# Kernel tuning notes

Measured on AMD Instinct MI355X. Metric: run time of the kernel, lower is better.

The kernel has to match this reference:

```python
import jax, jax.numpy as jnp
import numpy as np

N_NODES = 100000
N_EDGES = 1600000
D_IN = 128
D_OUT = 128
NEG_SLOPE = 0.01  # torch F.leaky_relu default


def setup_inputs() -> dict:
    key = jax.random.key(0)
    k1, k2, k3, k4, k5 = jax.random.split(key, 5)
    h = jax.random.normal(k1, (N_NODES, D_IN), dtype=jnp.float32)
    # nn.Linear default init scale ~ 1/sqrt(fan_in)
    W = jax.random.normal(k2, (D_IN, D_OUT), dtype=jnp.float32) / np.sqrt(D_IN)
    attn_w = jax.random.normal(k3, (2 * D_OUT,), dtype=jnp.float32) / np.sqrt(2 * D_OUT)
    edge_src = jax.random.randint(k4, (N_EDGES,), 0, N_NODES, dtype=jnp.int32)
    edge_dst = jax.random.randint(k5, (N_EDGES,), 0, N_NODES, dtype=jnp.int32)
    return {"h": h, "W": W, "attn_w": attn_w, "edge_src": edge_src, "edge_dst": edge_dst}


def reference(h, W, attn_w, edge_src, edge_dst):
    n = h.shape[0]
    d = W.shape[1]
    z = h @ W                                   # [N, d]
    # attention_func(cat([z_src, z_dst])) == z_src @ a[:d] + z_dst @ a[d:]
    s_src = z @ attn_w[:d]                      # [N]
    s_dst = z @ attn_w[d:]                      # [N]
    e = jax.nn.leaky_relu(s_src[edge_src] + s_dst[edge_dst], NEG_SLOPE)  # [E]
    # segment softmax over incoming edges of each dst node
    m = jax.ops.segment_max(e, edge_dst, num_segments=n)   # [N], -inf for empty
    ex = jnp.exp(e - m[edge_dst])                           # [E]
    denom = jax.ops.segment_sum(ex, edge_dst, num_segments=n)  # [N]
    alpha = ex / denom[edge_dst]                             # [E]
    # weighted neighbor sum: sum_j alpha_ij * z_j
    out = jax.ops.segment_sum(alpha[:, None] * z[edge_src], edge_dst, num_segments=n)
    return out
```

## Files before the change

### kernel.cpp

```cpp
#include <hip/hip_runtime.h>

#define D 128
#define NEG_SLOPE 0.01f
#define BSHIFT 7
#define B1 1024
#define STR 136
#define SCHUNK 4096
#define SLOT 2560

typedef __attribute__((ext_vector_type(8))) short short8;
typedef __attribute__((ext_vector_type(4))) float floatx4;

__device__ __forceinline__ unsigned f2bf_rne(float x) {
    unsigned u = __float_as_uint(x);
    return (u + 0x7fffu + ((u >> 16) & 1u)) >> 16;
}
#define BF_LO(u) __uint_as_float((u) << 16)
#define BF_HI(u) __uint_as_float((u) & 0xffff0000u)

__global__ void init_gcur(int* __restrict__ gcur) {
    const int i = threadIdx.x;
    gcur[i] = i * SLOT;
}

__global__ __launch_bounds__(1024) void sort_scatter(const int* __restrict__ esrc,
                                                     const int* __restrict__ edst,
                                                     int* __restrict__ gcur,
                                                     int* __restrict__ pairs, int E) {
    __shared__ int cnt[B1], exc[B1], gbs[B1], cur[B1];
    __shared__ int spk[SCHUNK];
    __shared__ unsigned short sbkt[SCHUNK];
    const int t = threadIdx.x;
    cnt[t] = 0; cur[t] = 0;
    __syncthreads();

    const int e0 = blockIdx.x * SCHUNK;
    const int n  = min(SCHUNK, E - e0);

    int pk[4], bk[4];
#pragma unroll
    for (int k = 0; k < 4; ++k) {
        const int i = t + k * 1024;
        if (i < n) {
            const int d = edst[e0 + i];
            const int s = esrc[e0 + i];
            bk[k] = d >> BSHIFT;
            pk[k] = (s << BSHIFT) | (d & 127);
            atomicAdd(&cnt[bk[k]], 1);
        } else {
            bk[k] = -1;
        }
    }
    __syncthreads();

    exc[t] = cnt[t];
    __syncthreads();
    for (int off = 1; off < B1; off <<= 1) {
        int v = (t >= off) ? exc[t - off] : 0;
        __syncthreads();
        exc[t] += v;
        __syncthreads();
    }
    const int myexc = exc[t] - cnt[t];
    exc[t] = myexc;
    if (cnt[t] > 0) gbs[t] = atomicAdd(&gcur[t], cnt[t]);
    __syncthreads();

#pragma unroll
    for (int k = 0; k < 4; ++k) {
        if (bk[k] >= 0) {
            const int p = exc[bk[k]] + atomicAdd(&cur[bk[k]], 1);
            spk[p]  = pk[k];
            sbkt[p] = (unsigned short)bk[k];
        }
    }
    __syncthreads();

    for (int i = t; i < n; i += 1024) {
        const int b = sbkt[i];
        const int pos = gbs[b] + (i - exc[b]);
        if (pos < (b + 1) * SLOT) pairs[pos] = spk[i];
    }
}

__global__ __launch_bounds__(256) void fine_build(const int* __restrict__ pairs,
                                                  const int* __restrict__ gcur,
                                                  int* __restrict__ beg,
                                                  int* __restrict__ ncnt,
                                                  int* __restrict__ adj, int N) {
    __shared__ int cnt[128], sc[128], cur[128];
    const int b = blockIdx.x;
    const int base = b << BSHIFT;
    const int nd = min(128, N - base);
    const int t = threadIdx.x;
    const int s0 = b * SLOT;
    const int e1 = min(gcur[b], s0 + SLOT);
    if (t < 128) { cnt[t] = 0; cur[t] = 0; }
    __syncthreads();
    for (int i = s0 + t; i < e1; i += 256)
        atomicAdd(&cnt[pairs[i] & 127], 1);
    __syncthreads();
    if (t < 128) sc[t] = cnt[t];
    __syncthreads();
    for (int off = 1; off < 128; off <<= 1) {
        int v = (t < 128 && t >= off) ? sc[t - off] : 0;
        __syncthreads();
        if (t < 128) sc[t] += v;
        __syncthreads();
    }
    if (t < nd) {
        beg[base + t]  = s0 + sc[t] - cnt[t];
        ncnt[base + t] = cnt[t];
    }
    __syncthreads();
    for (int i = s0 + t; i < e1; i += 256) {
        const int pkv = pairs[i];
        const int d = pkv & 127;
        const int pos = s0 + (sc[d] - cnt[d]) + atomicAdd(&cur[d], 1);
        adj[pos] = pkv >> BSHIFT;
    }
}

__global__ __launch_bounds__(256) void gemm_zs(const float* __restrict__ h,
                                               const float* __restrict__ W,
                                               const float* __restrict__ aw,
                                               unsigned short* __restrict__ z,
                                               float* __restrict__ s_src,
                                               float* __restrict__ s_dst, int N) {
    __shared__ unsigned short ws_hi[D * STR];
    __shared__ unsigned short ws_lo[D * STR];
    const int t = threadIdx.x;
    for (int i = t; i < D * D; i += 256) {
        int k = i >> 7, n = i & 127;
        float x = W[i];
        unsigned hi = f2bf_rne(x);
        float hf = __uint_as_float(hi << 16);
        unsigned lo = __float_as_uint(x - hf) >> 16;
        ws_hi[n * STR + k] = (unsigned short)hi;
        ws_lo[n * STR + k] = (unsigned short)lo;
    }
    __syncthreads();

    const int lane = t & 63, quad = lane >> 4, l16 = lane & 15;
    const int rowbase = blockIdx.x * 64 + (t >> 6) * 16;
    const int arow = min(rowbase + l16, N - 1);
    const float* __restrict__ hrow = h + (size_t)arow * D;

    floatx4 acc[8];
#pragma unroll
    for (int ct = 0; ct < 8; ++ct) acc[ct] = (floatx4){0.f, 0.f, 0.f, 0.f};

#pragma unroll
    for (int kk = 0; kk < 4; ++kk) {
        const int k0 = kk * 32 + quad * 8;
        float4 x0 = *(const float4*)&hrow[k0];
        float4 x1 = *(const float4*)&hrow[k0 + 4];
        float xs[8] = {x0.x, x0.y, x0.z, x0.w, x1.x, x1.y, x1.z, x1.w};
        union { short8 v; unsigned short u[8]; } ahi, alo;
#pragma unroll
        for (int i = 0; i < 8; ++i) {
            unsigned hi = f2bf_rne(xs[i]);
            float hf = __uint_as_float(hi << 16);
            ahi.u[i] = (unsigned short)hi;
            alo.u[i] = (unsigned short)(__float_as_uint(xs[i] - hf) >> 16);
        }
#pragma unroll
        for (int ct = 0; ct < 8; ++ct) {
            const int bo = (ct * 16 + l16) * STR + k0;
            short8 bhi = *(const short8*)&ws_hi[bo];
            short8 blo = *(const short8*)&ws_lo[bo];
            acc[ct] = __builtin_amdgcn_mfma_f32_16x16x32_bf16(ahi.v, bhi, acc[ct], 0, 0, 0);
            acc[ct] = __builtin_amdgcn_mfma_f32_16x16x32_bf16(alo.v, bhi, acc[ct], 0, 0, 0);
            acc[ct] = __builtin_amdgcn_mfma_f32_16x16x32_bf16(ahi.v, blo, acc[ct], 0, 0, 0);
        }
    }

#pragma unroll
    for (int ct = 0; ct < 8; ++ct)
#pragma unroll
        for (int reg = 0; reg < 4; ++reg) {
            int r = rowbase + quad * 4 + reg;
            if (r < N)
                z[(size_t)r * D + ct * 16 + l16] = (unsigned short)f2bf_rne(acc[ct][reg]);
        }

    float ps[4] = {0.f, 0.f, 0.f, 0.f}, pd[4] = {0.f, 0.f, 0.f, 0.f};
#pragma unroll
    for (int ct = 0; ct < 8; ++ct) {
        float as = aw[ct * 16 + l16];
        float ad = aw[128 + ct * 16 + l16];
#pragma unroll
        for (int reg = 0; reg < 4; ++reg) {
            ps[reg] = fmaf(acc[ct][reg], as, ps[reg]);
            pd[reg] = fmaf(acc[ct][reg], ad, pd[reg]);
        }
    }
#pragma unroll
    for (int reg = 0; reg < 4; ++reg)
#pragma unroll
        for (int o = 1; o < 16; o <<= 1) {
            ps[reg] += __shfl_xor(ps[reg], o, 64);
            pd[reg] += __shfl_xor(pd[reg], o, 64);
        }
    if (l16 == 0) {
#pragma unroll
        for (int reg = 0; reg < 4; ++reg) {
            int r = rowbase + quad * 4 + reg;
            if (r < N) { s_src[r] = ps[reg]; s_dst[r] = pd[reg]; }
        }
    }
}

__global__ __launch_bounds__(256) void aggregate(const unsigned short* __restrict__ z,
                                                 const float* __restrict__ s_src,
                                                 const float* __restrict__ s_dst,
                                                 const int* __restrict__ beg_,
                                                 const int* __restrict__ ncnt_,
                                                 const int* __restrict__ adj,
                                                 float* __restrict__ out, int N) {
    const int lane = threadIdx.x & 63;
    const int q    = lane >> 4;
    const int l16  = lane & 15;
    const int node = blockIdx.x * 4 + (threadIdx.x >> 6);
    if (node >= N) return;
    const int beg = beg_[node];
    const int cnt = ncnt_[node];
    const float sd = s_dst[node];

    float a[8] = {0.f,0.f,0.f,0.f,0.f,0.f,0.f,0.f};
    float bacc[8] = {0.f,0.f,0.f,0.f,0.f,0.f,0.f,0.f};

    auto fma8 = [&](float* ac, float w, const uint4& v) {
        ac[0] = fmaf(w, BF_LO(v.x), ac[0]); ac[1] = fmaf(w, BF_HI(v.x), ac[1]);
        ac[2] = fmaf(w, BF_LO(v.y), ac[2]); ac[3] = fmaf(w, BF_HI(v.y), ac[3]);
        ac[4] = fmaf(w, BF_LO(v.z), ac[4]); ac[5] = fmaf(w, BF_HI(v.z), ac[5]);
        ac[6] = fmaf(w, BF_LO(v.w), ac[6]); ac[7] = fmaf(w, BF_HI(v.w), ac[7]);
    };

    if (cnt <= 64) {
        int s = 0; float e = -INFINITY;
        if (lane < cnt) {
            s = adj[beg + lane];
            float t = s_src[s] + sd;
            e = (t >= 0.f) ? t : NEG_SLOPE * t;
        }
        int sj[4]; uint4 zv[4];
#pragma unroll
        for (int u = 0; u < 4; ++u) sj[u] = __shfl(s, u * 4 + q, 64);
#pragma unroll
        for (int u = 0; u < 4; ++u)
            zv[u] = *(const uint4*)&z[(size_t)sj[u] * D + l16 * 8];

        float mx = e;
#pragma unroll
        for (int o = 32; o; o >>= 1) mx = fmaxf(mx, __shfl_xor(mx, o, 64));
        float ex = (lane < cnt) ? __expf(e - mx) : 0.f;
        float sum = ex;
#pragma unroll
        for (int o = 32; o; o >>= 1) sum += __shfl_xor(sum, o, 64);
        const float inv = (cnt > 0) ? 1.f / sum : 0.f;
        const float w = ex * inv;

#pragma unroll
        for (int u = 0; u < 4; ++u) {
            const int ji = u * 4 + q;
            float wj = __shfl(w, ji, 64);
            wj = (ji < cnt) ? wj : 0.f;
            fma8((u & 1) ? bacc : a, wj, zv[u]);
        }
        for (int jj = 16; jj < cnt; jj += 16) {
            int ji2[4]; float wj[4]; int sj2[4];
#pragma unroll
            for (int u = 0; u < 4; ++u) {
                ji2[u] = jj + u * 4 + q;
                wj[u]  = __shfl(w, ji2[u], 64);
                sj2[u] = __shfl(s, ji2[u], 64);
                wj[u]  = (ji2[u] < cnt) ? wj[u] : 0.f;
            }
            uint4 z0 = *(const uint4*)&z[(size_t)sj2[0] * D + l16 * 8];
            uint4 z1 = *(const uint4*)&z[(size_t)sj2[1] * D + l16 * 8];
            uint4 z2 = *(const uint4*)&z[(size_t)sj2[2] * D + l16 * 8];
            uint4 z3 = *(const uint4*)&z[(size_t)sj2[3] * D + l16 * 8];
            fma8(a, wj[0], z0);
            fma8(bacc, wj[1], z1);
            fma8(a, wj[2], z2);
            fma8(bacc, wj[3], z3);
        }
    } else {
        float mx = -INFINITY;
        for (int j = lane; j < cnt; j += 64) {
            float t = s_src[adj[beg + j]] + sd;
            t = (t >= 0.f) ? t : NEG_SLOPE * t;
            mx = fmaxf(mx, t);
        }
#pragma unroll
        for (int o = 32; o; o >>= 1) mx = fmaxf(mx, __shfl_xor(mx, o, 64));
        float sum = 0.f;
        for (int j = lane; j < cnt; j += 64) {
            float t = s_src[adj[beg + j]] + sd;
            t = (t >= 0.f) ? t : NEG_SLOPE * t;
            sum += __expf(t - mx);
        }
#pragma unroll
        for (int o = 32; o; o >>= 1) sum += __shfl_xor(sum, o, 64);
        const float inv = 1.f / sum;
        for (int base2 = 0; base2 < cnt; base2 += 64) {
            const int cc = min(64, cnt - base2);
            int s = 0; float w = 0.f;
            if (lane < cc) {
                s = adj[beg + base2 + lane];
                float t = s_src[s] + sd;
                t = (t >= 0.f) ? t : NEG_SLOPE * t;
                w = __expf(t - mx) * inv;
            }
            for (int jj = 0; jj < cc; jj += 8) {
                const int ja = jj + q;
                const int jb = ja + 4;
                float wa = __shfl(w, ja, 64); int sa = __shfl(s, ja, 64);
                float wb = __shfl(w, jb, 64); int sb = __shfl(s, jb, 64);
                wa = (ja < cc) ? wa : 0.f;
                wb = (jb < cc) ? wb : 0.f;
                uint4 za = *(const uint4*)&z[(size_t)sa * D + l16 * 8];
                uint4 zb = *(const uint4*)&z[(size_t)sb * D + l16 * 8];
                fma8(a, wa, za);
                fma8(bacc, wb, zb);
            }
        }
    }

#pragma unroll
    for (int i = 0; i < 8; ++i) {
        a[i] += bacc[i];
        a[i] += __shfl_xor(a[i], 16, 64);
        a[i] += __shfl_xor(a[i], 32, 64);
    }
    if (q == 0) {
        float* o = &out[(size_t)node * D + l16 * 8];
        *(float4*)o       = make_float4(a[0], a[1], a[2], a[3]);
        *(float4*)(o + 4) = make_float4(a[4], a[5], a[6], a[7]);
    }
}

extern "C" void kernel_launch(void* const* d_in, const int* in_sizes, int n_in,
                              void* d_out, int out_size, void* d_ws, size_t ws_size,
                              hipStream_t stream) {
    const float* h    = (const float*)d_in[0];
    const float* W    = (const float*)d_in[1];
    const float* aw   = (const float*)d_in[2];
    const int*   esrc = (const int*)d_in[3];
    const int*   edst = (const int*)d_in[4];
    float* out = (float*)d_out;

    const int N = in_sizes[0] / D;
    const int E = in_sizes[3];
    const int NB1   = (N + 127) >> BSHIFT;
    const int NSORT = (E + SCHUNK - 1) / SCHUNK;

    char* p = (char*)d_ws;
    auto carve = [&](size_t bytes) {
        void* r = (void*)p;
        p += (bytes + 255) & ~size_t(255);
        return r;
    };
    unsigned short* z = (unsigned short*)carve(size_t(N) * D * sizeof(unsigned short));
    float* s_src  = (float*)carve(size_t(N) * sizeof(float));
    float* s_dst  = (float*)carve(size_t(N) * sizeof(float));
    int*   pairs  = (int*)carve(size_t(NB1) * SLOT * sizeof(int));
    int*   adj    = (int*)carve(size_t(NB1) * SLOT * sizeof(int));
    int*   beg    = (int*)carve(size_t(N) * sizeof(int));
    int*   ncnt   = (int*)carve(size_t(N) * sizeof(int));
    int*   gcur   = (int*)carve(size_t(B1) * sizeof(int));
    (void)ws_size; (void)n_in; (void)out_size;

    init_gcur<<<1, B1, 0, stream>>>(gcur);
    sort_scatter<<<NSORT, 1024, 0, stream>>>(esrc, edst, gcur, pairs, E);
    fine_build<<<NB1, 256, 0, stream>>>(pairs, gcur, beg, ncnt, adj, N);
    gemm_zs<<<(N + 63) / 64, 256, 0, stream>>>(h, W, aw, z, s_src, s_dst, N);
    aggregate<<<(N + 3) / 4, 256, 0, stream>>>(z, s_src, s_dst, beg, ncnt, adj, out, N);
}
```

Baseline: 232.5 us.

## Pack two nodes per wavefront in aggregate and streamline sort/build kernels

The aggregate kernel now gives each wavefront two destination nodes, one per 32-lane half, when both have at most 32 incoming edges. Large-degree nodes fall back to processing the pair sequentially. This targets lane waste, since the average in-degree is about 16. The sort_scatter kernel moves to 512 threads with 6 edges per thread and swaps the 1024-step shared-memory scan for a wavefront shuffle scan. fine_build reads pairs into registers once instead of twice, using a fixed 10-slot unroll that relies on SLOT being 2560.

Measured after the change: 241.3 us. 1.04x slower.

```diff
diff --git a/kernel.cpp b/kernel.cpp
--- a/kernel.cpp
+++ b/kernel.cpp
@@ -5,7 +5,8 @@
 #define BSHIFT 7
 #define B1 1024
 #define STR 136
-#define SCHUNK 4096
+#define SCHUNK 3072
+#define SEPT 6
 #define SLOT 2560
 
 typedef __attribute__((ext_vector_type(8))) short short8;
@@ -23,24 +24,25 @@
     gcur[i] = i * SLOT;
 }
 
-__global__ __launch_bounds__(1024) void sort_scatter(const int* __restrict__ esrc,
-                                                     const int* __restrict__ edst,
-                                                     int* __restrict__ gcur,
-                                                     int* __restrict__ pairs, int E) {
+__global__ __launch_bounds__(512) void sort_scatter(const int* __restrict__ esrc,
+                                                    const int* __restrict__ edst,
+                                                    int* __restrict__ gcur,
+                                                    int* __restrict__ pairs, int E) {
     __shared__ int cnt[B1], exc[B1], gbs[B1], cur[B1];
     __shared__ int spk[SCHUNK];
     __shared__ unsigned short sbkt[SCHUNK];
+    __shared__ int wtot[8];
     const int t = threadIdx.x;
-    cnt[t] = 0; cur[t] = 0;
+    cnt[t] = 0; cnt[t + 512] = 0; cur[t] = 0; cur[t + 512] = 0;
     __syncthreads();
 
     const int e0 = blockIdx.x * SCHUNK;
     const int n  = min(SCHUNK, E - e0);
 
-    int pk[4], bk[4];
-#pragma unroll
-    for (int k = 0; k < 4; ++k) {
-        const int i = t + k * 1024;
+    int pk[SEPT], bk[SEPT];
+#pragma unroll
+    for (int k = 0; k < SEPT; ++k) {
+        const int i = t + k * 512;
         if (i < n) {
             const int d = edst[e0 + i];
             const int s = esrc[e0 + i];
@@ -53,21 +55,29 @@
     }
     __syncthreads();
 
-    exc[t] = cnt[t];
-    __syncthreads();
-    for (int off = 1; off < B1; off <<= 1) {
-        int v = (t >= off) ? exc[t - off] : 0;
-        __syncthreads();
-        exc[t] += v;
-        __syncthreads();
-    }
-    const int myexc = exc[t] - cnt[t];
-    exc[t] = myexc;
-    if (cnt[t] > 0) gbs[t] = atomicAdd(&gcur[t], cnt[t]);
-    __syncthreads();
-
-#pragma unroll
-    for (int k = 0; k < 4; ++k) {
+    const int c0 = cnt[2 * t], c1 = cnt[2 * t + 1];
+    const int s2 = c0 + c1;
+    int incl = s2;
+#pragma unroll
+    for (int o = 1; o < 64; o <<= 1) {
+        int v = __shfl_up(incl, o, 64);
+        if ((t & 63) >= o) incl += v;
+    }
+    const int wv = t >> 6;
+    if ((t & 63) == 63) wtot[wv] = incl;
+    __syncthreads();
+    int wpre = 0;
+#pragma unroll
+    for (int i = 0; i < 8; ++i) wpre += (i < wv) ? wtot[i] : 0;
+    const int ex0 = wpre + incl - s2;
+    exc[2 * t]     = ex0;
+    exc[2 * t + 1] = ex0 + c0;
+    if (c0 > 0) gbs[2 * t]     = atomicAdd(&gcur[2 * t], c0);
+    if (c1 > 0) gbs[2 * t + 1] = atomicAdd(&gcur[2 * t + 1], c1);
+    __syncthreads();
+
+#pragma unroll
+    for (int k = 0; k < SEPT; ++k) {
         if (bk[k] >= 0) {
             const int p = exc[bk[k]] + atomicAdd(&cur[bk[k]], 1);
             spk[p]  = pk[k];
@@ -76,7 +86,7 @@
     }
     __syncthreads();
 
-    for (int i = t; i < n; i += 1024) {
+    for (int i = t; i < n; i += 512) {
         const int b = sbkt[i];
         const int pos = gbs[b] + (i - exc[b]);
         if (pos < (b + 1) * SLOT) pairs[pos] = spk[i];
@@ -97,8 +107,13 @@
     const int e1 = min(gcur[b], s0 + SLOT);
     if (t < 128) { cnt[t] = 0; cur[t] = 0; }
     __syncthreads();
-    for (int i = s0 + t; i < e1; i += 256)
-        atomicAdd(&cnt[pairs[i] & 127], 1);
+    int pk[10];
+#pragma unroll
+    for (int k = 0; k < 10; ++k) {
+        const int i = s0 + t + k * 256;
+        pk[k] = (i < e1) ? pairs[i] : -1;
+        if (pk[k] >= 0) atomicAdd(&cnt[pk[k] & 127], 1);
+    }
     __syncthreads();
     if (t < 128) sc[t] = cnt[t];
     __syncthreads();
@@ -113,11 +128,13 @@
         ncnt[base + t] = cnt[t];
     }
     __syncthreads();
-    for (int i = s0 + t; i < e1; i += 256) {
-        const int pkv = pairs[i];
-        const int d = pkv & 127;
-        const int pos = s0 + (sc[d] - cnt[d]) + atomicAdd(&cur[d], 1);
-        adj[pos] = pkv >> BSHIFT;
+#pragma unroll
+    for (int k = 0; k < 10; ++k) {
+        if (pk[k] >= 0) {
+            const int d = pk[k] & 127;
+            const int pos = s0 + (sc[d] - cnt[d]) + atomicAdd(&cur[d], 1);
+            adj[pos] = pk[k] >> BSHIFT;
+        }
     }
 }
 
@@ -219,16 +236,17 @@
                                                  const int* __restrict__ adj,
                                                  float* __restrict__ out, int N) {
     const int lane = threadIdx.x & 63;
-    const int q    = lane >> 4;
+    const int half = lane >> 5;
+    const int l32  = lane & 31;
+    const int q2   = l32 >> 4;
     const int l16  = lane & 15;
-    const int node = blockIdx.x * 4 + (threadIdx.x >> 6);
-    if (node >= N) return;
-    const int beg = beg_[node];
-    const int cnt = ncnt_[node];
-    const float sd = s_dst[node];
-
-    float a[8] = {0.f,0.f,0.f,0.f,0.f,0.f,0.f,0.f};
-    float bacc[8] = {0.f,0.f,0.f,0.f,0.f,0.f,0.f,0.f};
+    const int hb   = half << 5;
+    const int pairBase = blockIdx.x * 8 + (threadIdx.x >> 6) * 2;
+    if (pairBase >= N) return;
+    const int nodeA = pairBase, nodeB = pairBase + 1;
+    const int cA = ncnt_[nodeA], bA = beg_[nodeA];
+    int cB = 0, bB = 0;
+    if (nodeB < N) { cB = ncnt_[nodeB]; bB = beg_[nodeB]; }
 
     auto fma8 = [&](float* ac, float w, const uint4& v) {
         ac[0] = fmaf(w, BF_LO(v.x), ac[0]); ac[1] = fmaf(w, BF_HI(v.x), ac[1]);
@@ -237,45 +255,51 @@
         ac[6] = fmaf(w, BF_LO(v.w), ac[6]); ac[7] = fmaf(w, BF_HI(v.w), ac[7]);
     };
 
-    if (cnt <= 64) {
+    if (max(cA, cB) <= 32) {
+        const int myn = pairBase + half;
+        const int mb  = half ? bB : bA;
+        const int mc  = half ? cB : cA;
+        const float sd = s_dst[myn < N ? myn : 0];
         int s = 0; float e = -INFINITY;
-        if (lane < cnt) {
-            s = adj[beg + lane];
-            float t = s_src[s] + sd;
-            e = (t >= 0.f) ? t : NEG_SLOPE * t;
+        if (l32 < mc) {
+            s = adj[mb + l32];
+            float tt = s_src[s] + sd;
+            e = (tt >= 0.f) ? tt : NEG_SLOPE * tt;
         }
         int sj[4]; uint4 zv[4];
 #pragma unroll
-        for (int u = 0; u < 4; ++u) sj[u] = __shfl(s, u * 4 + q, 64);
+        for (int u = 0; u < 4; ++u) sj[u] = __shfl(s, hb + u * 2 + q2, 64);
 #pragma unroll
         for (int u = 0; u < 4; ++u)
             zv[u] = *(const uint4*)&z[(size_t)sj[u] * D + l16 * 8];
 
         float mx = e;
 #pragma unroll
-        for (int o = 32; o; o >>= 1) mx = fmaxf(mx, __shfl_xor(mx, o, 64));
-        float ex = (lane < cnt) ? __expf(e - mx) : 0.f;
+        for (int o = 16; o; o >>= 1) mx = fmaxf(mx, __shfl_xor(mx, o, 64));
+        float ex = (l32 < mc) ? __expf(e - mx) : 0.f;
         float sum = ex;
 #pragma unroll
-        for (int o = 32; o; o >>= 1) sum += __shfl_xor(sum, o, 64);
-        const float inv = (cnt > 0) ? 1.f / sum : 0.f;
+        for (int o = 16; o; o >>= 1) sum += __shfl_xor(sum, o, 64);
+        const float inv = (mc > 0) ? 1.f / sum : 0.f;
         const float w = ex * inv;
 
+        float a[8] = {0.f,0.f,0.f,0.f,0.f,0.f,0.f,0.f};
+        float bacc[8] = {0.f,0.f,0.f,0.f,0.f,0.f,0.f,0.f};
 #pragma unroll
         for (int u = 0; u < 4; ++u) {
-            const int ji = u * 4 + q;
-            float wj = __shfl(w, ji, 64);
-            wj = (ji < cnt) ? wj : 0.f;
+            const int ji = u * 2 + q2;
+            float wj = __shfl(w, hb + ji, 64);
+            wj = (ji < mc) ? wj : 0.f;
             fma8((u & 1) ? bacc : a, wj, zv[u]);
         }
-        for (int jj = 16; jj < cnt; jj += 16) {
+        for (int jj = 8; jj < mc; jj += 8) {
             int ji2[4]; float wj[4]; int sj2[4];
 #pragma unroll
             for (int u = 0; u < 4; ++u) {
-                ji2[u] = jj + u * 4 + q;
-                wj[u]  = __shfl(w, ji2[u], 64);
-                sj2[u] = __shfl(s, ji2[u], 64);
-                wj[u]  = (ji2[u] < cnt) ? wj[u] : 0.f;
+                ji2[u] = jj + u * 2 + q2;
+                wj[u]  = __shfl(w, hb + ji2[u], 64);
+                sj2[u] = __shfl(s, hb + ji2[u], 64);
+                wj[u]  = (ji2[u] < mc) ? wj[u] : 0.f;
             }
             uint4 z0 = *(const uint4*)&z[(size_t)sj2[0] * D + l16 * 8];
             uint4 z1 = *(const uint4*)&z[(size_t)sj2[1] * D + l16 * 8];
@@ -286,32 +310,53 @@
             fma8(a, wj[2], z2);
             fma8(bacc, wj[3], z3);
         }
-    } else {
+#pragma unroll
+        for (int i = 0; i < 8; ++i) {
+            a[i] += bacc[i];
+            a[i] += __shfl_xor(a[i], 16, 64);
+        }
+        if (q2 == 0 && myn < N) {
+            float* o = &out[(size_t)myn * D + l16 * 8];
+            *(float4*)o       = make_float4(a[0], a[1], a[2], a[3]);
+            *(float4*)(o + 4) = make_float4(a[4], a[5], a[6], a[7]);
+        }
+        return;
+    }
+
+    const int q = lane >> 4;
+    for (int which = 0; which < 2; ++which) {
+        const int myn = which ? nodeB : nodeA;
+        if (myn >= N) break;
+        const int mb = which ? bB : bA;
+        const int mc = which ? cB : cA;
+        const float sd = s_dst[myn];
+        float a[8] = {0.f,0.f,0.f,0.f,0.f,0.f,0.f,0.f};
+        float bacc[8] = {0.f,0.f,0.f,0.f,0.f,0.f,0.f,0.f};
         float mx = -INFINITY;
-        for (int j = lane; j < cnt; j += 64) {
-            float t = s_src[adj[beg + j]] + sd;
-            t = (t >= 0.f) ? t : NEG_SLOPE * t;
-            mx = fmaxf(mx, t);
+        for (int j = lane; j < mc; j += 64) {
+            float tt = s_src[adj[mb + j]] + sd;
+            tt = (tt >= 0.f) ? tt : NEG_SLOPE * tt;
+            mx = fmaxf(mx, tt);
         }
 #pragma unroll
         for (int o = 32; o; o >>= 1) mx = fmaxf(mx, __shfl_xor(mx, o, 64));
         float sum = 0.f;
-        for (int j = lane; j < cnt; j += 64) {
-            float t = s_src[adj[beg + j]] + sd;
-            t = (t >= 0.f) ? t : NEG_SLOPE * t;
-            sum += __expf(t - mx);
+        for (int j = lane; j < mc; j += 64) {
+            float tt = s_src[adj[mb + j]] + sd;
+            tt = (tt >= 0.f) ? tt : NEG_SLOPE * tt;
+            sum += __expf(tt - mx);
         }
 #pragma unroll
         for (int o = 32; o; o >>= 1) sum += __shfl_xor(sum, o, 64);
-        const float inv = 1.f / sum;
-        for (int base2 = 0; base2 < cnt; base2 += 64) {
-            const int cc = min(64, cnt - base2);
+        const float inv = (mc > 0) ? 1.f / sum : 0.f;
+        for (int base2 = 0; base2 < mc; base2 += 64) {
+            const int cc = min(64, mc - base2);
             int s = 0; float w = 0.f;
             if (lane < cc) {
-                s = adj[beg + base2 + lane];
-                float t = s_src[s] + sd;
-                t = (t >= 0.f) ? t : NEG_SLOPE * t;
-                w = __expf(t - mx) * inv;
+                s = adj[mb + base2 + lane];
+                float tt = s_src[s] + sd;
+                tt = (tt >= 0.f) ? tt : NEG_SLOPE * tt;
+                w = __expf(tt - mx) * inv;
             }
             for (int jj = 0; jj < cc; jj += 8) {
                 const int ja = jj + q;
@@ -326,18 +371,17 @@
                 fma8(bacc, wb, zb);
             }
         }
-    }
-
-#pragma unroll
-    for (int i = 0; i < 8; ++i) {
-        a[i] += bacc[i];
-        a[i] += __shfl_xor(a[i], 16, 64);
-        a[i] += __shfl_xor(a[i], 32, 64);
-    }
-    if (q == 0) {
-        float* o = &out[(size_t)node * D + l16 * 8];
-        *(float4*)o       = make_float4(a[0], a[1], a[2], a[3]);
-        *(float4*)(o + 4) = make_float4(a[4], a[5], a[6], a[7]);
+#pragma unroll
+        for (int i = 0; i < 8; ++i) {
+            a[i] += bacc[i];
+            a[i] += __shfl_xor(a[i], 16, 64);
+            a[i] += __shfl_xor(a[i], 32, 64);
+        }
+        if (q == 0) {
+            float* o = &out[(size_t)myn * D + l16 * 8];
+            *(float4*)o       = make_float4(a[0], a[1], a[2], a[3]);
+            *(float4*)(o + 4) = make_float4(a[4], a[5], a[6], a[7]);
+        }
     }
 }
 
@@ -373,8 +417,8 @@
     (void)ws_size; (void)n_in; (void)out_size;
 
     init_gcur<<<1, B1, 0, stream>>>(gcur);
-    sort_scatter<<<NSORT, 1024, 0, stream>>>(esrc, edst, gcur, pairs, E);
+    sort_scatter<<<NSORT, 512, 0, stream>>>(esrc, edst, gcur, pairs, E);
     fine_build<<<NB1, 256, 0, stream>>>(pairs, gcur, beg, ncnt, adj, N);
     gemm_zs<<<(N + 63) / 64, 256, 0, stream>>>(h, W, aw, z, s_src, s_dst, N);
-    aggregate<<<(N + 3) / 4, 256, 0, stream>>>(z, s_src, s_dst, beg, ncnt, adj, out, N);
-}
+    aggregate<<<(N + 7) / 8, 256, 0, stream>>>(z, s_src, s_dst, beg, ncnt, adj, out, N);
+}
```
